# Kernel tuning notes

Hardware: AMD Instinct MI355X
Metric: run time of the kernel (lower is better)

## Reference

```python
import jax, jax.numpy as jnp
import numpy as np

B, S, E, H = 2, 2048, 1024, 16
HD = E // H


def setup_inputs() -> dict:
    key = jax.random.key(0)
    ks = jax.random.split(key, 5)
    scale = 1.0 / np.sqrt(E)
    return {
        "x": jax.random.normal(ks[0], (B, S, E), dtype=jnp.float32),
        "Wq": jax.random.normal(ks[1], (H, HD, E), dtype=jnp.float32) * scale,
        "Wk": jax.random.normal(ks[2], (H, HD, E), dtype=jnp.float32) * scale,
        "Wv": jax.random.normal(ks[3], (H, HD, E), dtype=jnp.float32) * scale,
        "Wo": jax.random.normal(ks[4], (E, E), dtype=jnp.float32) * scale,
    }


def reference(x, Wq, Wk, Wv, Wo):
    # Batched per-head projections: torch Linear y = x @ W.T, W: [head_dim, E]
    q = jnp.einsum("bse,hde->bshd", x, Wq)  # [B,S,H,HD]
    k = jnp.einsum("bse,hde->bshd", x, Wk)
    v = jnp.einsum("bse,hde->bshd", x, Wv)
    # Scaled dot-product attention; original scales by sqrt(head_dim)
    scores = jnp.einsum("bqhd,bkhd->bhqk", q, k) / jnp.sqrt(jnp.float32(HD))
    attn = jax.nn.softmax(scores, axis=-1)  # [B,H,S,S]
    out_h = jnp.einsum("bhqk,bkhd->bqhd", attn, v)  # [B,S,H,HD]
    out_cat = out_h.reshape(x.shape[0], x.shape[1], -1)  # concat heads -> [B,S,E]
    return out_cat @ Wo.T
```

## Files before the change

### kernel.cpp

```cpp
#include <hip/hip_runtime.h>
#include <hip/hip_bf16.h>

typedef unsigned short u16;
typedef unsigned int u32;
typedef __attribute__((ext_vector_type(4))) float f32x4;
typedef __attribute__((ext_vector_type(8))) short short8;
typedef __attribute__((ext_vector_type(8))) unsigned short u16x8;
typedef __attribute__((ext_vector_type(4))) unsigned short u16x4;
typedef __attribute__((ext_vector_type(2))) unsigned int u32x2;

#define BATCH 2
#define SEQ   2048
#define EMB   1024
#define NH    16
#define HD    64

__device__ inline u16 f2bf(float f) {
    unsigned u = __builtin_bit_cast(unsigned, f);
    unsigned r = u + 0x7FFFu + ((u >> 16) & 1u);
    return (u16)(r >> 16);
}

__device__ inline float fexp2(float x) {
    float r;
    asm("v_exp_f32 %0, %1" : "=v"(r) : "v"(x));
    return r;
}

__device__ inline void gload16(const void* g, void* l) {
    __builtin_amdgcn_global_load_lds(
        (const __attribute__((address_space(1))) unsigned int*)g,
        (__attribute__((address_space(3))) unsigned int*)l, 16, 0, 0);
}

__global__ __launch_bounds__(256) void convert_all(
    const float* __restrict__ x,
    const float* __restrict__ Wq, const float* __restrict__ Wk, const float* __restrict__ Wv,
    u16* __restrict__ Xb, u16* __restrict__ Wqkv)
{
    const long gidx = (long)blockIdx.x * 2048 + (long)threadIdx.x * 8;
    const float* src;
    u16* dst;
    if (gidx < 4194304L) {
        src = x + gidx; dst = Xb + gidx;
    } else {
        const long r = gidx - 4194304L;
        const int w = (int)(r >> 20);
        const long off = r & 1048575L;
        src = (w == 0 ? Wq : w == 1 ? Wk : Wv) + off;
        dst = Wqkv + r;
    }
    f32x4 a = *(const f32x4*)src;
    f32x4 b = *(const f32x4*)(src + 4);
    u16x8 o;
    #pragma unroll
    for (int j = 0; j < 4; ++j) { o[j] = f2bf(a[j]); o[4 + j] = f2bf(b[j]); }
    *(u16x8*)dst = o;
}

__global__ __launch_bounds__(256) void convert_wo(
    const float* __restrict__ Wo, u16* __restrict__ Wob)
{
    const long gidx = (long)blockIdx.x * 2048 + (long)threadIdx.x * 8;
    f32x4 a = *(const f32x4*)(Wo + gidx);
    f32x4 b = *(const f32x4*)(Wo + gidx + 4);
    u16x8 o;
    #pragma unroll
    for (int j = 0; j < 4; ++j) { o[j] = f2bf(a[j]); o[4 + j] = f2bf(b[j]); }
    *(u16x8*)(Wob + gidx) = o;
}

__global__ __launch_bounds__(512, 2) void gemm256(
    const u16* __restrict__ A, const u16* __restrict__ Bb,
    u16* __restrict__ Qo, u16* __restrict__ Ko, u16* __restrict__ VTo)
{
    __shared__ u16 As[2][256 * 64];
    __shared__ u16 Bs[2][256 * 64];

    const int tid = threadIdx.x;
    const int lane = tid & 63;
    const int wid = tid >> 6;
    const int lr = lane & 15;
    const int lg = lane >> 4;
    const int wr = wid >> 2;
    const int wc = wid & 3;
    const int m0 = blockIdx.x * 256;
    const int n0 = blockIdx.y * 256;

    const int grow = lane >> 3;
    const int schunk = ((lane & 7) ^ grow) << 4;

    auto issueTile = [&](int kt, int buf) {
        const int k0b = kt * 128;
        #pragma unroll
        for (int i = 0; i < 4; ++i) {
            const int row = i * 64 + wid * 8 + grow;
            gload16((const char*)A + (size_t)(m0 + row) * 2048 + k0b + schunk,
                    (char*)As[buf] + i * 8192 + wid * 1024);
            gload16((const char*)Bb + (size_t)(n0 + row) * 2048 + k0b + schunk,
                    (char*)Bs[buf] + i * 8192 + wid * 1024);
        }
    };

    issueTile(0, 0);
    issueTile(1, 1);

    f32x4 acc[8][4] = {};
    const int rsw = (lr & 7);

    for (int t = 0; t < 16; ++t) {
        if (t < 15) { asm volatile("s_waitcnt vmcnt(8)" ::: "memory"); }
        else        { asm volatile("s_waitcnt vmcnt(0)" ::: "memory"); }
        __builtin_amdgcn_sched_barrier(0);
        __builtin_amdgcn_s_barrier();
        __builtin_amdgcn_sched_barrier(0);

        const u16* Ac = As[t & 1];
        const u16* Bc = Bs[t & 1];

        short8 a[4][2], b0[2][2], b1[2][2];

        #pragma unroll
        for (int fi = 0; fi < 4; ++fi)
            #pragma unroll
            for (int ks = 0; ks < 2; ++ks)
                a[fi][ks] = *(const short8*)((const char*)Ac + (wr * 128 + fi * 16 + lr) * 128
                                             + (((ks * 4 + lg) ^ rsw) << 4));
        #pragma unroll
        for (int fj = 0; fj < 2; ++fj)
            #pragma unroll
            for (int ks = 0; ks < 2; ++ks)
                b0[fj][ks] = *(const short8*)((const char*)Bc + (wc * 64 + fj * 16 + lr) * 128
                                              + (((ks * 4 + lg) ^ rsw) << 4));
        __builtin_amdgcn_s_setprio(1);
        #pragma unroll
        for (int fi = 0; fi < 4; ++fi)
            #pragma unroll
            for (int fj = 0; fj < 2; ++fj)
                #pragma unroll
                for (int ks = 0; ks < 2; ++ks)
                    acc[fi][fj] = __builtin_amdgcn_mfma_f32_16x16x32_bf16(a[fi][ks], b0[fj][ks], acc[fi][fj], 0, 0, 0);
        __builtin_amdgcn_s_setprio(0);

        #pragma unroll
        for (int fj = 0; fj < 2; ++fj)
            #pragma unroll
            for (int ks = 0; ks < 2; ++ks)
                b1[fj][ks] = *(const short8*)((const char*)Bc + (wc * 64 + (fj + 2) * 16 + lr) * 128
                                              + (((ks * 4 + lg) ^ rsw) << 4));
        __builtin_amdgcn_s_setprio(1);
        #pragma unroll
        for (int fi = 0; fi < 4; ++fi)
            #pragma unroll
            for (int fj = 0; fj < 2; ++fj)
                #pragma unroll
                for (int ks = 0; ks < 2; ++ks)
                    acc[fi][fj + 2] = __builtin_amdgcn_mfma_f32_16x16x32_bf16(a[fi][ks], b1[fj][ks], acc[fi][fj + 2], 0, 0, 0);
        __builtin_amdgcn_s_setprio(0);

        #pragma unroll
        for (int fi = 0; fi < 4; ++fi)
            #pragma unroll
            for (int ks = 0; ks < 2; ++ks)
                a[fi][ks] = *(const short8*)((const char*)Ac + (wr * 128 + (fi + 4) * 16 + lr) * 128
                                             + (((ks * 4 + lg) ^ rsw) << 4));
        __builtin_amdgcn_s_setprio(1);
        #pragma unroll
        for (int fi = 0; fi < 4; ++fi)
            #pragma unroll
            for (int fj = 0; fj < 2; ++fj)
                #pragma unroll
                for (int ks = 0; ks < 2; ++ks)
                    acc[fi + 4][fj + 2] = __builtin_amdgcn_mfma_f32_16x16x32_bf16(a[fi][ks], b1[fj][ks], acc[fi + 4][fj + 2], 0, 0, 0);
        __builtin_amdgcn_s_setprio(0);

        __builtin_amdgcn_s_setprio(1);
        #pragma unroll
        for (int fi = 0; fi < 4; ++fi)
            #pragma unroll
            for (int fj = 0; fj < 2; ++fj)
                #pragma unroll
                for (int ks = 0; ks < 2; ++ks)
                    acc[fi + 4][fj] = __builtin_amdgcn_mfma_f32_16x16x32_bf16(a[fi][ks], b0[fj][ks], acc[fi + 4][fj], 0, 0, 0);
        __builtin_amdgcn_s_setprio(0);

        __builtin_amdgcn_sched_barrier(0);
        __builtin_amdgcn_s_barrier();
        __builtin_amdgcn_sched_barrier(0);
        if (t + 2 < 16) issueTile(t + 2, t & 1);
    }

    const int w = n0 >> 10;
    const float qs = (w == 0) ? 0.125f * 1.44269504f : 1.0f;
    const int mb = m0 + wr * 128;
    const int nb = n0 + wc * 64;
    #pragma unroll
    for (int fi = 0; fi < 8; ++fi) {
        #pragma unroll
        for (int fj = 0; fj < 4; ++fj) {
            const int m = mb + fi * 16 + lg * 4;
            const int nn = (nb + fj * 16 + lr) & 1023;
            const int h = nn >> 6, d = nn & 63;
            const int bb = m >> 11, s = m & 2047;
            const size_t bh = (size_t)(bb * NH + h);
            if (w == 2) {
                u16x4 v;
                #pragma unroll
                for (int i = 0; i < 4; ++i) v[i] = f2bf(acc[fi][fj][i]);
                *(u16x4*)&VTo[(bh * HD + d) * SEQ + s] = v;
            } else {
                u16* P = (w == 0) ? Qo : Ko;
                #pragma unroll
                for (int i = 0; i < 4; ++i)
                    P[(bh * SEQ + s + i) * HD + d] = f2bf(acc[fi][fj][i] * qs);
            }
        }
    }
}

template<int MODE>
__global__ __launch_bounds__(256) void gemm_bt(
    const u16* __restrict__ A, const u16* __restrict__ Bb,
    u16* __restrict__ Qo, u16* __restrict__ Ko, u16* __restrict__ VTo,
    float* __restrict__ Fo)
{
    __shared__ u16 As[2][128 * 64];
    __shared__ u16 Bs[2][128 * 64];

    const int tid = threadIdx.x;
    const int m0 = blockIdx.x * 128;
    const int n0 = blockIdx.y * 128;

    const int lane = tid & 63;
    const int lr = lane & 15;
    const int lg = lane >> 4;
    const int wid = tid >> 6;
    const int wm = wid >> 1, wn = wid & 1;

    const int grow = lane >> 3;
    const int gcolb = ((lane & 7) ^ grow) << 4;
    const int rswz = (lr & 7);

    f32x4 acc[4][4] = {};

    auto issue = [&](int kt, int buf) {
        const int k0b = kt * 128;
        #pragma unroll
        for (int t = 0; t < 4; ++t) {
            const int row = (wid * 4 + t) * 8 + grow;
            gload16((const char*)A + (size_t)(m0 + row) * 2048 + k0b + gcolb,
                    (char*)As[buf] + (wid * 4 + t) * 1024);
            gload16((const char*)Bb + (size_t)(n0 + row) * 2048 + k0b + gcolb,
                    (char*)Bs[buf] + (wid * 4 + t) * 1024);
        }
    };

    issue(0, 0);

    for (int kt = 0; kt < 16; ++kt) {
        const int cur = kt & 1;
        __syncthreads();
        if (kt + 1 < 16) issue(kt + 1, cur ^ 1);

        const u16* Ac = As[cur];
        const u16* Bc = Bs[cur];
        #pragma unroll
        for (int kk = 0; kk < 2; ++kk) {
            short8 a[4], b[4];
            #pragma unroll
            for (int i = 0; i < 4; ++i)
                a[i] = *(const short8*)((const char*)Ac + (wm * 64 + i * 16 + lr) * 128
                                        + (((kk * 4 + lg) ^ rswz) << 4));
            #pragma unroll
            for (int i = 0; i < 4; ++i)
                b[i] = *(const short8*)((const char*)Bc + (wn * 64 + i * 16 + lr) * 128
                                        + (((kk * 4 + lg) ^ rswz) << 4));
            #pragma unroll
            for (int mi = 0; mi < 4; ++mi)
                #pragma unroll
                for (int ni = 0; ni < 4; ++ni)
                    acc[mi][ni] = __builtin_amdgcn_mfma_f32_16x16x32_bf16(a[mi], b[ni], acc[mi][ni], 0, 0, 0);
        }
    }

    const int mb = m0 + wm * 64;
    const int nb = n0 + wn * 64;
    #pragma unroll
    for (int mi = 0; mi < 4; ++mi)
        #pragma unroll
        for (int ni = 0; ni < 4; ++ni) {
            const int m = mb + mi * 16 + lg * 4;
            const int n = nb + ni * 16 + lr;
            #pragma unroll
            for (int i = 0; i < 4; ++i)
                Fo[(size_t)(m + i) * EMB + n] = acc[mi][ni][i];
        }
}

__global__ __launch_bounds__(512) void attn_fwd(
    const u16* __restrict__ Q, const u16* __restrict__ K,
    const u16* __restrict__ VT, u16* __restrict__ Cat)
{
    __shared__ u16 Ks[2][64 * 64];
    __shared__ u16 Vs[2][80 * 64];
    __shared__ u16 PT[8][16 * 72];

    const int tid = threadIdx.x;
    const int lane = tid & 63;
    const int lr = lane & 15;
    const int lg = lane >> 4;
    const int wid = tid >> 6;
    const int qt = blockIdx.x;
    const int bh = blockIdx.y;
    const int b = bh >> 4, h = bh & 15;

    if (tid < 128) {
        const int row = 64 + (tid >> 3), sl = tid & 7;
        u16x8 ones;
        #pragma unroll
        for (int j = 0; j < 8; ++j) ones[j] = 0x3F80;
        *(u16x8*)((char*)Vs[0] + row * 128 + ((sl ^ (row & 7)) << 4)) = ones;
        *(u16x8*)((char*)Vs[1] + row * 128 + ((sl ^ (row & 7)) << 4)) = ones;
    }

    const u16* Qg = Q + ((size_t)bh * SEQ + qt * 128 + wid * 16 + lr) * HD;
    short8 qf[2];
    qf[0] = *(const short8*)(Qg + lg * 8);
    qf[1] = *(const short8*)(Qg + 32 + lg * 8);

    float m = -1e30f;
    f32x4 accO[5] = {};

    const u16* Kg = K + (size_t)bh * SEQ * HD;
    const u16* Vg = VT + (size_t)bh * HD * SEQ;

    const int srow = lane >> 3;
    const int schunk = ((lane & 7) ^ srow) << 4;

    auto issueKV = [&](int nt, int buf) {
        const int kv0 = nt * 64;
        const int krow = wid * 8 + srow;
        gload16((const char*)Kg + (size_t)(kv0 + krow) * 128 + schunk,
                (char*)Ks[buf] + wid * 1024);
        gload16((const char*)Vg + (size_t)krow * (SEQ * 2) + kv0 * 2 + schunk,
                (char*)Vs[buf] + wid * 1024);
    };

    issueKV(0, 0);

    for (int nt = 0; nt < SEQ / 64; ++nt) {
        const int cur = nt & 1;
        __syncthreads();
        if (nt + 1 < SEQ / 64) issueKV(nt + 1, cur ^ 1);

        f32x4 st[4] = {};
        #pragma unroll
        for (int kk = 0; kk < 2; ++kk) {
            const short8 qv = qf[kk];
            #pragma unroll
            for (int c = 0; c < 4; ++c) {
                const short8 kf = *(const short8*)((const char*)Ks[cur] + (c * 16 + lr) * 128
                                                   + (((kk * 4 + lg) ^ (lr & 7)) << 4));
                st[c] = __builtin_amdgcn_mfma_f32_16x16x32_bf16(kf, qv, st[c], 0, 0, 0);
            }
        }

        float mx = fmaxf(
            fmaxf(fmaxf(fmaxf(st[0][0], st[0][1]), fmaxf(st[0][2], st[0][3])),
                  fmaxf(fmaxf(st[1][0], st[1][1]), fmaxf(st[1][2], st[1][3]))),
            fmaxf(fmaxf(fmaxf(st[2][0], st[2][1]), fmaxf(st[2][2], st[2][3])),
                  fmaxf(fmaxf(st[3][0], st[3][1]), fmaxf(st[3][2], st[3][3]))));
        mx = fmaxf(mx, __shfl_xor(mx, 16));
        mx = fmaxf(mx, __shfl_xor(mx, 32));
        if (!__all(mx - m <= 11.5f)) {
            const float nm = fmaxf(m, mx);
            const float corr = fexp2(m - nm);
            m = nm;
            #pragma unroll
            for (int dc = 0; dc < 5; ++dc)
                accO[dc] *= corr;
        }
        #pragma unroll
        for (int c = 0; c < 4; ++c)
            #pragma unroll
            for (int i = 0; i < 4; ++i)
                st[c][i] = fexp2(st[c][i] - m);

        #pragma unroll
        for (int c = 0; c < 4; ++c) {
            u32 w0, w1;
            asm("v_cvt_pk_bf16_f32 %0, %1, %2" : "=v"(w0) : "v"(st[c][0]), "v"(st[c][1]));
            asm("v_cvt_pk_bf16_f32 %0, %1, %2" : "=v"(w1) : "v"(st[c][2]), "v"(st[c][3]));
            u32x2 pk; pk[0] = w0; pk[1] = w1;
            *(u32x2*)&PT[wid][lr * 72 + c * 16 + lg * 4] = pk;
        }
        asm volatile("s_waitcnt lgkmcnt(0)" ::: "memory");
        __builtin_amdgcn_sched_barrier(0);

        #pragma unroll
        for (int kk = 0; kk < 2; ++kk) {
            const short8 pf = *(const short8*)&PT[wid][lr * 72 + kk * 32 + lg * 8];
            #pragma unroll
            for (int dc = 0; dc < 5; ++dc) {
                const short8 vf = *(const short8*)((const char*)Vs[cur] + (dc * 16 + lr) * 128
                                                   + (((kk * 4 + lg) ^ (lr & 7)) << 4));
                accO[dc] = __builtin_amdgcn_mfma_f32_16x16x32_bf16(vf, pf, accO[dc], 0, 0, 0);
            }
        }
    }

    const float invl = 1.f / accO[4][0];
    const int qs = qt * 128 + wid * 16 + lr;
    u16* ob = Cat + (size_t)b * SEQ * EMB + (size_t)qs * EMB + h * HD;
    #pragma unroll
    for (int dc = 0; dc < 4; ++dc) {
        u16x4 o;
        #pragma unroll
        for (int i = 0; i < 4; ++i) o[i] = f2bf(accO[dc][i] * invl);
        *(u16x4*)&ob[dc * 16 + lg * 4] = o;
    }
}

extern "C" void kernel_launch(void* const* d_in, const int* in_sizes, int n_in,
                              void* d_out, int out_size, void* d_ws, size_t ws_size,
                              hipStream_t stream) {
    const float* x  = (const float*)d_in[0];
    const float* Wq = (const float*)d_in[1];
    const float* Wk = (const float*)d_in[2];
    const float* Wv = (const float*)d_in[3];
    const float* Wo = (const float*)d_in[4];
    float* out = (float*)d_out;

    u16* Xb   = (u16*)d_out;
    u16* Wqkv = (u16*)d_out + (size_t)4 * 1048576;

    char* ws = (char*)d_ws;
    u16* Qb  = (u16*)(ws);
    u16* Kb  = (u16*)(ws + (size_t)8  * 1048576);
    u16* VTb = (u16*)(ws + (size_t)16 * 1048576);
    u16* Cat = (u16*)(ws + (size_t)24 * 1048576);
    u16* Wob = Qb;

    convert_all<<<3584, 256, 0, stream>>>(x, Wq, Wk, Wv, Xb, Wqkv);

    dim3 g1(4096 / 256, 3072 / 256);
    gemm256<<<g1, 512, 0, stream>>>(Xb, Wqkv, Qb, Kb, VTb);

    dim3 g2(SEQ / 128, BATCH * NH);
    attn_fwd<<<g2, 512, 0, stream>>>(Qb, Kb, VTb, Cat);

    convert_wo<<<512, 256, 0, stream>>>(Wo, Wob);
    dim3 g3(4096 / 128, 1024 / 128);
    gemm_bt<1><<<g3, 256, 0, stream>>>(Cat, Wob, nullptr, nullptr, nullptr, out);
}
```

Measured before the change: 126.0 us.

## Deepen prefetch to two tiles with explicit vmcnt waits and swizzle block order

The output GEMM and attention kernels now prefetch two tiles ahead. Each uses explicit s_waitcnt vmcnt counts plus raw barriers in place of __syncthreads, and a trailing barrier protects buffer reuse before the next load. This is meant to hide global-load latency behind MFMA work. Block indices in the QKV GEMM and attention kernels are also remapped so neighbouring blocks spread across XCDs for better cache locality. The costs are an extra barrier per iteration and hand-tuned wait counts that must match the number of outstanding loads.

```diff
diff --git a/kernel.cpp b/kernel.cpp
--- a/kernel.cpp
+++ b/kernel.cpp
@@ -84,8 +84,11 @@
     const int lg = lane >> 4;
     const int wr = wid >> 2;
     const int wc = wid & 3;
-    const int m0 = blockIdx.x * 256;
-    const int n0 = blockIdx.y * 256;
+
+    const int lin = blockIdx.y * 16 + blockIdx.x;
+    const int swz = (lin & 7) * 24 + (lin >> 3);
+    const int m0 = (swz & 15) * 256;
+    const int n0 = (swz >> 4) * 256;
 
     const int grow = lane >> 3;
     const int schunk = ((lane & 7) ^ grow) << 4;
@@ -218,11 +221,8 @@
     }
 }
 
-template<int MODE>
-__global__ __launch_bounds__(256) void gemm_bt(
-    const u16* __restrict__ A, const u16* __restrict__ Bb,
-    u16* __restrict__ Qo, u16* __restrict__ Ko, u16* __restrict__ VTo,
-    float* __restrict__ Fo)
+__global__ __launch_bounds__(256) void gemm_out(
+    const u16* __restrict__ A, const u16* __restrict__ Bb, float* __restrict__ Fo)
 {
     __shared__ u16 As[2][128 * 64];
     __shared__ u16 Bs[2][128 * 64];
@@ -256,14 +256,17 @@
     };
 
     issue(0, 0);
+    issue(1, 1);
 
     for (int kt = 0; kt < 16; ++kt) {
-        const int cur = kt & 1;
-        __syncthreads();
-        if (kt + 1 < 16) issue(kt + 1, cur ^ 1);
-
-        const u16* Ac = As[cur];
-        const u16* Bc = Bs[cur];
+        if (kt < 15) { asm volatile("s_waitcnt vmcnt(8)" ::: "memory"); }
+        else         { asm volatile("s_waitcnt vmcnt(0)" ::: "memory"); }
+        __builtin_amdgcn_sched_barrier(0);
+        __builtin_amdgcn_s_barrier();
+        __builtin_amdgcn_sched_barrier(0);
+
+        const u16* Ac = As[kt & 1];
+        const u16* Bc = Bs[kt & 1];
         #pragma unroll
         for (int kk = 0; kk < 2; ++kk) {
             short8 a[4], b[4];
@@ -281,6 +284,11 @@
                 for (int ni = 0; ni < 4; ++ni)
                     acc[mi][ni] = __builtin_amdgcn_mfma_f32_16x16x32_bf16(a[mi], b[ni], acc[mi][ni], 0, 0, 0);
         }
+
+        __builtin_amdgcn_sched_barrier(0);
+        __builtin_amdgcn_s_barrier();
+        __builtin_amdgcn_sched_barrier(0);
+        if (kt + 2 < 16) issue(kt + 2, kt & 1);
     }
 
     const int mb = m0 + wm * 64;
@@ -310,8 +318,11 @@
     const int lr = lane & 15;
     const int lg = lane >> 4;
     const int wid = tid >> 6;
-    const int qt = blockIdx.x;
-    const int bh = blockIdx.y;
+
+    const int lin = blockIdx.y * 16 + blockIdx.x;
+    const int swz = (lin & 7) * 64 + (lin >> 3);
+    const int qt = swz & 15;
+    const int bh = swz >> 4;
     const int b = bh >> 4, h = bh & 15;
 
     if (tid < 128) {
@@ -322,6 +333,7 @@
         *(u16x8*)((char*)Vs[0] + row * 128 + ((sl ^ (row & 7)) << 4)) = ones;
         *(u16x8*)((char*)Vs[1] + row * 128 + ((sl ^ (row & 7)) << 4)) = ones;
     }
+    asm volatile("s_waitcnt lgkmcnt(0)" ::: "memory");
 
     const u16* Qg = Q + ((size_t)bh * SEQ + qt * 128 + wid * 16 + lr) * HD;
     short8 qf[2];
@@ -347,11 +359,16 @@
     };
 
     issueKV(0, 0);
-
-    for (int nt = 0; nt < SEQ / 64; ++nt) {
+    issueKV(1, 1);
+
+    const int NT = SEQ / 64;
+    for (int nt = 0; nt < NT; ++nt) {
         const int cur = nt & 1;
-        __syncthreads();
-        if (nt + 1 < SEQ / 64) issueKV(nt + 1, cur ^ 1);
+        if (nt < NT - 1) { asm volatile("s_waitcnt vmcnt(2)" ::: "memory"); }
+        else             { asm volatile("s_waitcnt vmcnt(0)" ::: "memory"); }
+        __builtin_amdgcn_sched_barrier(0);
+        __builtin_amdgcn_s_barrier();
+        __builtin_amdgcn_sched_barrier(0);
 
         f32x4 st[4] = {};
         #pragma unroll
@@ -407,6 +424,11 @@
                 accO[dc] = __builtin_amdgcn_mfma_f32_16x16x32_bf16(vf, pf, accO[dc], 0, 0, 0);
             }
         }
+
+        __builtin_amdgcn_sched_barrier(0);
+        __builtin_amdgcn_s_barrier();
+        __builtin_amdgcn_sched_barrier(0);
+        if (nt + 2 < NT) issueKV(nt + 2, cur);
     }
 
     const float invl = 1.f / accO[4][0];
@@ -451,5 +473,5 @@
 
     convert_wo<<<512, 256, 0, stream>>>(Wo, Wob);
     dim3 g3(4096 / 128, 1024 / 128);
-    gemm_bt<1><<<g3, 256, 0, stream>>>(Cat, Wob, nullptr, nullptr, nullptr, out);
-}
+    gemm_out<<<g3, 256, 0, stream>>>(Cat, Wob, out);
+}
```

Result: no change. 126.2 us (+0.1%).
